# Kernel optimization log

Hardware: AMD Instinct MI355X
Metric: run time of the kernel (lower is better)

The kernel has to match this reference:

```python
import jax, jax.numpy as jnp
import numpy as np

EMBED_DIM = 1024
NUM_HEADS = 16
HEAD_DIM = EMBED_DIM // NUM_HEADS


def setup_inputs() -> dict:
    key = jax.random.key(0)
    k_x, k_wqkv, k_bqkv, k_wout, k_bout = jax.random.split(key, 5)
    s = 1.0 / np.sqrt(EMBED_DIM)
    return {
        "x": jax.random.normal(k_x, (2, 2048, EMBED_DIM), dtype=jnp.float32),
        "w_qkv": jax.random.uniform(k_wqkv, (EMBED_DIM, 3 * EMBED_DIM), jnp.float32, -s, s),
        "b_qkv": jax.random.uniform(k_bqkv, (3 * EMBED_DIM,), jnp.float32, -s, s),
        "w_out": jax.random.uniform(k_wout, (EMBED_DIM, EMBED_DIM), jnp.float32, -s, s),
        "b_out": jax.random.uniform(k_bout, (EMBED_DIM,), jnp.float32, -s, s),
    }


def reference(x, w_qkv, b_qkv, w_out, b_out):
    B, S, D = x.shape
    H, Hd = NUM_HEADS, HEAD_DIM
    # qkv projection, then per-head chunk: layout matches torch view(B,S,H,3*Hd).chunk(3,-1)
    qkv = (x @ w_qkv + b_qkv).reshape(B, S, H, 3, Hd)  # [B,S,H,3,Hd]
    q = qkv[..., 0, :]  # [B,S,H,Hd]
    k = qkv[..., 1, :]
    v = qkv[..., 2, :]
    scale = 1.0 / np.sqrt(Hd).astype(np.float32)
    scores = jnp.einsum("bqhd,bkhd->bhqk", q, k) * scale  # [B,H,S,S]
    probs = jax.nn.softmax(scores, axis=-1)
    out = jnp.einsum("bhqk,bkhd->bqhd", probs, v).reshape(B, S, D)
    return out @ w_out + b_out
```

## Files before the change

kernel.cpp:

```cpp
#include <hip/hip_runtime.h>
#include <hip/hip_bf16.h>


typedef __bf16 bf16;
typedef __bf16 bf16x8 __attribute__((ext_vector_type(8)));
typedef float  f32x4  __attribute__((ext_vector_type(4)));
typedef float  f32x16 __attribute__((ext_vector_type(16)));
typedef unsigned int uint;
typedef unsigned int uint2v __attribute__((ext_vector_type(2)));

__device__ __forceinline__ void gload_lds16(const void* g, void* l) {
  __builtin_amdgcn_global_load_lds(
      (const __attribute__((address_space(1))) unsigned int*)g,
      (__attribute__((address_space(3))) unsigned int*)l, 16, 0, 0);
}

__device__ __forceinline__ uint pkbf16(float lo, float hi) {
  union { bf16 h[2]; uint u; } t;
  t.h[0] = (bf16)lo; t.h[1] = (bf16)hi;
  return t.u;
}

__device__ __forceinline__ void pl32swapu(uint& a, uint& b) {
  uint2v r = __builtin_amdgcn_permlane32_swap(a, b, false, false);
  a = r.x; b = r.y;
}
__device__ __forceinline__ void pl32swapf(float& a, float& b) {
  uint ua = __builtin_bit_cast(uint, a), ub = __builtin_bit_cast(uint, b);
  pl32swapu(ua, ub);
  a = __builtin_bit_cast(float, ua); b = __builtin_bit_cast(float, ub);
}

__global__ __launch_bounds__(256) void k_prep(const float* __restrict__ x,
                                              const float* __restrict__ w_qkv,
                                              const float* __restrict__ w_out,
                                              bf16* __restrict__ xb,
                                              bf16* __restrict__ wqT,
                                              bf16* __restrict__ woT) {
  __shared__ float tile[32][33];
  const int b = blockIdx.x;
  const int tid = threadIdx.x;
  if (b < 2048) {
    int i = (b * 256 + tid) * 8;
    float4 a = *(const float4*)(x + i);
    float4 c = *(const float4*)(x + i + 4);
    bf16x8 o;
    o[0] = (bf16)a.x; o[1] = (bf16)a.y; o[2] = (bf16)a.z; o[3] = (bf16)a.w;
    o[4] = (bf16)c.x; o[5] = (bf16)c.y; o[6] = (bf16)c.z; o[7] = (bf16)c.w;
    *(bf16x8*)(xb + i) = o;
    return;
  }
  const bool perm = (b < 5120);
  const float* in = perm ? w_qkv : w_out;
  bf16* out = perm ? wqT : woT;
  const int N = perm ? 3072 : 1024;
  int idx = perm ? (b - 2048) : (b - 5120);
  int gx = perm ? (idx % 96) : (idx % 32);
  int gy = perm ? (idx / 96) : (idx / 32);
  int n0 = gx * 32, k0 = gy * 32;
  int tx = tid & 31, ty = tid >> 5;
#pragma unroll
  for (int i = 0; i < 4; i++)
    tile[ty + i * 8][tx] = in[(size_t)(k0 + ty + i * 8) * N + n0 + tx];
  __syncthreads();
#pragma unroll
  for (int i = 0; i < 4; i++) {
    int n = n0 + ty + i * 8;
    int row = n;
    if (perm) {
      int rem = n % 192;
      row = (rem >> 6) * 1024 + (n / 192) * 64 + (rem & 63);
    }
    out[(size_t)row * 1024 + k0 + tx] = (bf16)tile[tx][ty + i * 8];
  }
}

template<int BM, int BN>
__device__ __forceinline__ void gemm_tile(const bf16* __restrict__ A, const bf16* __restrict__ B,
                                          int K, int m0, int n0,
                                          bf16* As, bf16* Bs, f32x4 acc[BM / 32][BN / 32]) {
  const int tid  = threadIdx.x;
  const int lane = tid & 63;
  const int wr   = (tid >> 7) & 1;
  const int wc   = (tid >> 6) & 1;
  constexpr int LA = BM / 64, LB = BN / 64;
  auto stage = [&](int k0v, int b) {
#pragma unroll
    for (int i = 0; i < LA; i++) {
      int row = i * 64 + (tid >> 2);
      int sw  = (tid & 3) ^ (row & 3);
      gload_lds16(A + (size_t)(m0 + row) * K + k0v + sw * 8, (char*)As + b * (BM * 64) + i * 4096 + tid * 16);
    }
#pragma unroll
    for (int i = 0; i < LB; i++) {
      int row = i * 64 + (tid >> 2);
      int sw  = (tid & 3) ^ (row & 3);
      gload_lds16(B + (size_t)(n0 + row) * K + k0v + sw * 8, (char*)Bs + b * (BN * 64) + i * 4096 + tid * 16);
    }
  };
  const int nk = K / 32;
  stage(0, 0); stage(32, 1); stage(64, 2);
  for (int t = 0; t < nk; t++) {
    if (t < nk - 2) {
      if constexpr (LA + LB == 4) asm volatile("s_waitcnt vmcnt(8)" ::: "memory");
      else                        asm volatile("s_waitcnt vmcnt(6)" ::: "memory");
    } else if (t < nk - 1) {
      if constexpr (LA + LB == 4) asm volatile("s_waitcnt vmcnt(4)" ::: "memory");
      else                        asm volatile("s_waitcnt vmcnt(3)" ::: "memory");
    } else {
      asm volatile("s_waitcnt vmcnt(0)" ::: "memory");
    }
    __builtin_amdgcn_s_barrier();
    asm volatile("" ::: "memory");
    if (t + 3 < nk) stage((t + 3) * 32, (t + 3) & 3);
    const int cur = t & 3;
    bf16x8 af[BM / 32], bfr[BN / 32];
#pragma unroll
    for (int r = 0; r < BM / 32; r++) {
      int ra = wr * (BM / 2) + r * 16 + (lane & 15);
      af[r]  = *(const bf16x8*)((const char*)As + cur * (BM * 64) + ra * 64 + ((((lane >> 4) << 4)) ^ ((ra & 3) << 4)));
    }
#pragma unroll
    for (int c = 0; c < BN / 32; c++) {
      int rb = wc * (BN / 2) + c * 16 + (lane & 15);
      bfr[c] = *(const bf16x8*)((const char*)Bs + cur * (BN * 64) + rb * 64 + ((((lane >> 4) << 4)) ^ ((rb & 3) << 4)));
    }
#pragma unroll
    for (int r = 0; r < BM / 32; r++)
#pragma unroll
      for (int c = 0; c < BN / 32; c++)
        acc[r][c] = __builtin_amdgcn_mfma_f32_16x16x32_bf16(af[r], bfr[c], acc[r][c], 0, 0, 0);
    asm volatile("" ::: "memory");
  }
}

__global__ __launch_bounds__(512, 2) void k_gemm_qkv(const bf16* __restrict__ A, const bf16* __restrict__ Bt,
                                                     const float* __restrict__ bias,
                                                     bf16* __restrict__ qb, char* __restrict__ kf,
                                                     char* __restrict__ vf) {
  __shared__ char GS[131072];
  const int tid  = threadIdx.x;
  const int lane = tid & 63;
  const int wave = tid >> 6;
  const int wr   = wave >> 2;
  const int wc   = wave & 3;
  const int l = blockIdx.x;
  const int swz = (l & 7) * 24 + (l >> 3);
  const int m0 = (swz / 12) * 256, n0 = (swz % 12) * 256;
  const int K = 1024;

  f32x4 acc[8][4];
  f32x4 zero = {0.f, 0.f, 0.f, 0.f};
#pragma unroll
  for (int ms = 0; ms < 8; ms++)
#pragma unroll
    for (int ns = 0; ns < 4; ns++) acc[ms][ns] = zero;

  const int ccs = tid & 7;
  int rA[2], rB[2];
  {
    int lr0 = tid >> 3;
    rA[0] = lr0;
    rB[0] = (lr0 & 31) + ((lr0 >> 5) << 6);
    int lr1 = 64 + lr0;
    rA[1] = (lr1 & 63) + 128;
    rB[1] = (lr1 & 31) + ((lr1 >> 5) << 6);
  }
  const bf16* Agp[2]; const bf16* Bgp[2];
  int Alo[2], Blo[2];
#pragma unroll
  for (int j = 0; j < 2; j++) {
    Agp[j] = A  + (size_t)(m0 + rA[j]) * K + (ccs ^ (rA[j] & 7)) * 8;
    Alo[j] = rA[j] * 128 + ccs * 16;
    Bgp[j] = Bt + (size_t)(n0 + rB[j]) * K + (ccs ^ (rB[j] & 7)) * 8;
    Blo[j] = rB[j] * 128 + ccs * 16;
  }
  auto stA = [&](int t, int h) {
    int b = t & 1;
#pragma unroll
    for (int j = 0; j < 2; j++)
      gload_lds16(Agp[j] + (size_t)(h * 64) * K + t * 64, GS + b * 32768 + Alo[j] + h * 8192);
  };
  auto stB = [&](int t, int h) {
    int b = t & 1;
#pragma unroll
    for (int j = 0; j < 2; j++)
      gload_lds16(Bgp[j] + (size_t)(h * 32) * K + t * 64, GS + 65536 + b * 32768 + Blo[j] + h * 4096);
  };

  bf16x8 af[4][2], bf0[2][2], bf1[2][2];
  auto rdA = [&](const char* Ab, int mh) {
#pragma unroll
    for (int ms = 0; ms < 4; ms++)
#pragma unroll
      for (int ks = 0; ks < 2; ks++) {
        int row = wr * 128 + (mh * 4 + ms) * 16 + (lane & 15);
        int ch = (ks * 4 + (lane >> 4)) ^ (row & 7);
        af[ms][ks] = *(const bf16x8*)(Ab + row * 128 + ch * 16);
      }
  };
  auto rdB = [&](const char* Bb, int nh, bf16x8 (&bfx)[2][2]) {
#pragma unroll
    for (int ns = 0; ns < 2; ns++)
#pragma unroll
      for (int ks = 0; ks < 2; ks++) {
        int row = wc * 64 + (nh * 2 + ns) * 16 + (lane & 15);
        int ch = (ks * 4 + (lane >> 4)) ^ (row & 7);
        bfx[ns][ks] = *(const bf16x8*)(Bb + row * 128 + ch * 16);
      }
  };
  auto mm = [&](int mh, int nh, bf16x8 (&bfx)[2][2]) {
    __builtin_amdgcn_s_setprio(1);
#pragma unroll
    for (int ks = 0; ks < 2; ks++)
#pragma unroll
      for (int ms = 0; ms < 4; ms++)
#pragma unroll
        for (int ns = 0; ns < 2; ns++)
          acc[mh * 4 + ms][nh * 2 + ns] =
              __builtin_amdgcn_mfma_f32_16x16x32_bf16(af[ms][ks], bfx[ns][ks],
                                                      acc[mh * 4 + ms][nh * 2 + ns], 0, 0, 0);
    __builtin_amdgcn_s_setprio(0);
  };

#define BARRIER do { asm volatile("" ::: "memory"); __builtin_amdgcn_s_barrier(); \
                     asm volatile("" ::: "memory"); } while (0)

  stA(0, 0); stB(0, 0); stB(0, 1); stA(0, 1);
  stA(1, 0); stB(1, 0); stB(1, 1);
  asm volatile("s_waitcnt vmcnt(6)" ::: "memory");
  __builtin_amdgcn_s_barrier();
  asm volatile("" ::: "memory");

  for (int I = 0; I < 8; I++) {
    const int T = 2 * I;
    const char* Ab0 = GS;
    const char* Bb0 = GS + 65536;
    const char* Ab1 = GS + 32768;
    const char* Bb1 = GS + 65536 + 32768;
    const bool m2 = (T + 2 < 16), m3 = (T + 3 < 16);

    rdA(Ab0, 0); rdB(Bb0, 0, bf0);
    stA(T + 1, 1);
    BARRIER;
    mm(0, 0, bf0);

    rdB(Bb0, 1, bf1);
    if (m2) stA(T + 2, 0);
    BARRIER;
    mm(0, 1, bf1);

    rdA(Ab0, 1);
    if (m2) stB(T + 2, 0);
    BARRIER;
    mm(1, 0, bf0);

    if (m2) {
      stB(T + 2, 1);
      asm volatile("s_waitcnt vmcnt(6)" ::: "memory");
    } else {
      asm volatile("s_waitcnt vmcnt(0)" ::: "memory");
    }
    __builtin_amdgcn_s_barrier();
    asm volatile("" ::: "memory");
    mm(1, 1, bf1);

    rdA(Ab1, 0); rdB(Bb1, 0, bf0);
    if (m2) stA(T + 2, 1);
    BARRIER;
    mm(0, 0, bf0);

    rdB(Bb1, 1, bf1);
    if (m3) stA(T + 3, 0);
    BARRIER;
    mm(0, 1, bf1);

    rdA(Ab1, 1);
    if (m3) stB(T + 3, 0);
    BARRIER;
    mm(1, 0, bf0);

    if (m3) {
      stB(T + 3, 1);
      asm volatile("s_waitcnt vmcnt(6)" ::: "memory");
    } else {
      asm volatile("s_waitcnt vmcnt(0)" ::: "memory");
    }
    __builtin_amdgcn_s_barrier();
    asm volatile("" ::: "memory");
    mm(1, 1, bf1);
  }
#undef BARRIER

  const int group = n0 >> 10;
  const int hb = (n0 & 1023) >> 6;
  const int b_ = m0 >> 11;
  const int kt0 = (m0 & 2047) >> 5;
  const float QSs = 0.125f * 1.4426950408889634f;
  char* TL = GS;

  if (group < 2) {
#pragma unroll
    for (int ms = 0; ms < 8; ms++) {
      int mloc = wr * 128 + ms * 16 + ((lane >> 4) << 2);
#pragma unroll
      for (int ns = 0; ns < 4; ns++) {
        int nloc = wc * 64 + ns * 16 + (lane & 15);
        int np = n0 + nloc;
        float bv = bias[((np & 1023) >> 6) * 192 + group * 64 + (np & 63)];
#pragma unroll
        for (int g = 0; g < 4; g++) {
          float v = acc[ms][ns][g] + bv;
          if (group == 0) v *= QSs;
          int m = mloc + g;
          int byte = m * 512 + ((((nloc >> 3) ^ (m & 7)) << 4) | ((nloc & 7) << 1));
          *(bf16*)(TL + byte) = (bf16)v;
        }
      }
    }
    __syncthreads();
    if (group == 0) {
#pragma unroll
      for (int it = 0; it < 16; it++) {
        int cid = it * 512 + tid;
        int row = cid >> 5, cc = cid & 31;
        int hh = hb + (cc >> 3), ck = cc & 7;
        bf16x8 v8 = *(const bf16x8*)(TL + row * 512 + ((cc ^ (row & 7)) << 4));
        *(bf16x8*)(qb + ((size_t)(b_ * 16 + hh) * 2048 + (m0 & 2047) + row) * 64 + ck * 8) = v8;
      }
    } else {
#pragma unroll
      for (int it = 0; it < 16; it++) {
        int cid = it * 512 + tid;
        int hh = cid >> 11;
        int ktl = (cid >> 8) & 7;
        int dc = (cid >> 6) & 3;
        int gg = (cid >> 5) & 1;
        int ln = cid & 31;
        int row = ktl * 32 + ln;
        int cc = hh * 8 + dc * 2 + gg;
        bf16x8 v8 = *(const bf16x8*)(TL + row * 512 + ((cc ^ (row & 7)) << 4));
        *(bf16x8*)(kf + ((size_t)(b_ * 16 + hb + hh) * 64 + kt0 + ktl) * 4096
                      + (dc * 2 + gg) * 512 + ln * 16) = v8;
      }
    }
  } else {
#pragma unroll
    for (int ms = 0; ms < 8; ms++) {
      int mloc = wr * 128 + ms * 16 + ((lane >> 4) << 2);
#pragma unroll
      for (int ns = 0; ns < 4; ns++) {
        int nloc = wc * 64 + ns * 16 + (lane & 15);
        int np = n0 + nloc;
        float bv = bias[((np & 1023) >> 6) * 192 + 2 * 64 + (np & 63)];
#pragma unroll
        for (int g = 0; g < 4; g++) {
          float v = acc[ms][ns][g] + bv;
          int m = mloc + g;
          int byte = nloc * 512 + ((((m >> 3) ^ (nloc & 7)) << 4) | ((m & 7) << 1));
          *(bf16*)(TL + byte) = (bf16)v;
        }
      }
    }
    __syncthreads();
#pragma unroll
    for (int it = 0; it < 16; it++) {
      int cid = it * 512 + tid;
      int hh = cid >> 11;
      int ktl = (cid >> 8) & 7;
      int kc = (cid >> 7) & 1;
      int dt = (cid >> 6) & 1;
      int gg = (cid >> 5) & 1;
      int ln = cid & 31;
      int row = hh * 64 + dt * 32 + ln;
      int mc = ktl * 4 + kc * 2 + gg;
      bf16x8 v8 = *(const bf16x8*)(TL + row * 512 + ((mc ^ (row & 7)) << 4));
      *(bf16x8*)(vf + ((size_t)(b_ * 16 + hb + hh) * 64 + kt0 + ktl) * 4096
                    + ((kc * 2 + dt) * 2 + gg) * 512 + ln * 16) = v8;
    }
  }
}

__global__ __launch_bounds__(256) void k_gemm_out(const bf16* __restrict__ A, const bf16* __restrict__ Bt,
                                                  const float* __restrict__ bias,
                                                  float* __restrict__ out) {
  __shared__ bf16 As[4 * 64 * 32];
  __shared__ bf16 Bs[4 * 128 * 32];
  const int l = blockIdx.x;
  const int swz = (l & 7) * 64 + (l >> 3);
  int m0 = (swz >> 3) * 64, n0 = (swz & 7) * 128;
  f32x4 zero = {0.f, 0.f, 0.f, 0.f};
  f32x4 acc[2][4];
#pragma unroll
  for (int r = 0; r < 2; r++)
#pragma unroll
    for (int c = 0; c < 4; c++) acc[r][c] = zero;
  gemm_tile<64, 128>(A, Bt, 1024, m0, n0, As, Bs, acc);
  const int lane = threadIdx.x & 63;
  const int wr = (threadIdx.x >> 7) & 1, wc = (threadIdx.x >> 6) & 1;
#pragma unroll
  for (int r = 0; r < 2; r++) {
    int mbase = m0 + wr * 32 + r * 16 + ((lane >> 4) << 2);
#pragma unroll
    for (int c = 0; c < 4; c++) {
      int n = n0 + wc * 64 + c * 16 + (lane & 15);
      float bv = bias[n];
#pragma unroll
      for (int g = 0; g < 4; g++)
        out[(size_t)(mbase + g) * 1024 + n] = acc[r][c][g] + bv;
    }
  }
}

__global__ __launch_bounds__(512, 2) void k_attn(const bf16* __restrict__ qb, const char* __restrict__ kf,
                                                 const char* __restrict__ vf, bf16* __restrict__ ob) {
  __shared__ char SMEM[73728];
  const int tid  = threadIdx.x;
  const int lane = tid & 63;
  const int wave = tid >> 6;
  const int qp   = wave & 3;
  const int half = wave >> 2;
  const int ln31 = lane & 31;
  const int g    = lane >> 5;

  int l = blockIdx.x;
  int x = l & 7, j = l >> 3;
  int qt = j & 7;
  int bh = x * 4 + (j >> 3);

  const int q0 = qt * 256 + qp * 64;

  bf16x8 qfa[4], qfb[4];
  {
    const bf16* qpa = qb + ((size_t)bh * 2048 + q0 + ln31) * 64 + g * 8;
    const bf16* qpb = qb + ((size_t)bh * 2048 + q0 + 32 + ln31) * 64 + g * 8;
#pragma unroll
    for (int dc = 0; dc < 4; dc++) {
      qfa[dc] = *(const bf16x8*)(qpa + dc * 16);
      qfb[dc] = *(const bf16x8*)(qpb + dc * 16);
    }
  }

  const f32x16 z16 = 0.f;
  f32x16 Oa0 = 0.f, Oa1 = 0.f, Ob0 = 0.f, Ob1 = 0.f;
  float lacc_a[4] = {0.f, 0.f, 0.f, 0.f};
  float lacc_b[4] = {0.f, 0.f, 0.f, 0.f};

  const int lb = (g * 32 + ln31) * 16;
  const char* Kp = kf + (size_t)bh * 262144 + (half * 32) * 4096 + lb;
  const char* Vp = vf + (size_t)bh * 262144 + (half * 32) * 4096 + lb;

  auto smx = [&](f32x16& sv, bf16x8& f0, bf16x8& f1, float (&lc)[4]) {
#pragma unroll
    for (int r = 0; r < 16; r++) sv[r] = __builtin_amdgcn_exp2f(sv[r]);
#pragma unroll
    for (int r = 0; r < 4; r++)
      lc[r] += (sv[r] + sv[r + 4]) + (sv[r + 8] + sv[r + 12]);
    uint a0 = pkbf16(sv[0], sv[1]), a1 = pkbf16(sv[2], sv[3]);
    uint a2 = pkbf16(sv[4], sv[5]), a3 = pkbf16(sv[6], sv[7]);
    pl32swapu(a0, a2); pl32swapu(a1, a3);
    union { uint w[4]; bf16x8 v; } pa;
    pa.w[0] = a0; pa.w[1] = a1; pa.w[2] = a2; pa.w[3] = a3;
    f0 = pa.v;
    uint b0 = pkbf16(sv[8], sv[9]),  b1 = pkbf16(sv[10], sv[11]);
    uint b2 = pkbf16(sv[12], sv[13]), b3 = pkbf16(sv[14], sv[15]);
    pl32swapu(b0, b2); pl32swapu(b1, b3);
    union { uint w[4]; bf16x8 v; } pb;
    pb.w[0] = b0; pb.w[1] = b1; pb.w[2] = b2; pb.w[3] = b3;
    f1 = pb.v;
  };

  bf16x8 k0 = *(const bf16x8*)(Kp +    0);
  bf16x8 k1 = *(const bf16x8*)(Kp + 1024);
  bf16x8 k2 = *(const bf16x8*)(Kp + 2048);
  bf16x8 k3 = *(const bf16x8*)(Kp + 3072);

  for (int ss = 0; ss < 32; ss++, Kp += 4096, Vp += 4096) {
    bf16x8 v00 = *(const bf16x8*)(Vp +    0);
    bf16x8 v01 = *(const bf16x8*)(Vp + 1024);
    bf16x8 v10 = *(const bf16x8*)(Vp + 2048);
    bf16x8 v11 = *(const bf16x8*)(Vp + 3072);
    bf16x8 n0 = *(const bf16x8*)(Kp + 4096);
    bf16x8 n1 = *(const bf16x8*)(Kp + 5120);
    bf16x8 n2 = *(const bf16x8*)(Kp + 6144);
    bf16x8 n3 = *(const bf16x8*)(Kp + 7168);

    f32x16 sa, sb;
    __builtin_amdgcn_s_setprio(1);
    sa = __builtin_amdgcn_mfma_f32_32x32x16_bf16(k0, qfa[0], z16, 0, 0, 0);
    sb = __builtin_amdgcn_mfma_f32_32x32x16_bf16(k0, qfb[0], z16, 0, 0, 0);
    sa = __builtin_amdgcn_mfma_f32_32x32x16_bf16(k1, qfa[1], sa, 0, 0, 0);
    sb = __builtin_amdgcn_mfma_f32_32x32x16_bf16(k1, qfb[1], sb, 0, 0, 0);
    sa = __builtin_amdgcn_mfma_f32_32x32x16_bf16(k2, qfa[2], sa, 0, 0, 0);
    sb = __builtin_amdgcn_mfma_f32_32x32x16_bf16(k2, qfb[2], sb, 0, 0, 0);
    sa = __builtin_amdgcn_mfma_f32_32x32x16_bf16(k3, qfa[3], sa, 0, 0, 0);
    sb = __builtin_amdgcn_mfma_f32_32x32x16_bf16(k3, qfb[3], sb, 0, 0, 0);
    __builtin_amdgcn_s_setprio(0);

    bf16x8 fa0, fa1, fb0, fb1;
    smx(sa, fa0, fa1, lacc_a);
    smx(sb, fb0, fb1, lacc_b);

    __builtin_amdgcn_s_setprio(1);
    Oa0 = __builtin_amdgcn_mfma_f32_32x32x16_bf16(v00, fa0, Oa0, 0, 0, 0);
    Ob0 = __builtin_amdgcn_mfma_f32_32x32x16_bf16(v00, fb0, Ob0, 0, 0, 0);
    Oa1 = __builtin_amdgcn_mfma_f32_32x32x16_bf16(v01, fa0, Oa1, 0, 0, 0);
    Ob1 = __builtin_amdgcn_mfma_f32_32x32x16_bf16(v01, fb0, Ob1, 0, 0, 0);
    Oa0 = __builtin_amdgcn_mfma_f32_32x32x16_bf16(v10, fa1, Oa0, 0, 0, 0);
    Ob0 = __builtin_amdgcn_mfma_f32_32x32x16_bf16(v10, fb1, Ob0, 0, 0, 0);
    Oa1 = __builtin_amdgcn_mfma_f32_32x32x16_bf16(v11, fa1, Oa1, 0, 0, 0);
    Ob1 = __builtin_amdgcn_mfma_f32_32x32x16_bf16(v11, fb1, Ob1, 0, 0, 0);
    __builtin_amdgcn_s_setprio(0);

    k0 = n0; k1 = n1; k2 = n2; k3 = n3;
  }

  float l_ra = (lacc_a[0] + lacc_a[1]) + (lacc_a[2] + lacc_a[3]);
  { float o = l_ra; pl32swapf(l_ra, o); l_ra += o; }
  float l_rb = (lacc_b[0] + lacc_b[1]) + (lacc_b[2] + lacc_b[3]);
  { float o = l_rb; pl32swapf(l_rb, o); l_rb += o; }

  float* Opart = (float*)SMEM;
  float* LsA   = (float*)(SMEM + 69632);
  float* LsB   = (float*)(SMEM + 70144);
  __syncthreads();
  if (half == 1) {
    float* my = Opart + (qp * 64 + lane) * 68;
#pragma unroll
    for (int c = 0; c < 4; c++) {
      *(f32x4*)(my +      c * 4) = f32x4{Oa0[c*4], Oa0[c*4+1], Oa0[c*4+2], Oa0[c*4+3]};
      *(f32x4*)(my + 16 + c * 4) = f32x4{Oa1[c*4], Oa1[c*4+1], Oa1[c*4+2], Oa1[c*4+3]};
      *(f32x4*)(my + 32 + c * 4) = f32x4{Ob0[c*4], Ob0[c*4+1], Ob0[c*4+2], Ob0[c*4+3]};
      *(f32x4*)(my + 48 + c * 4) = f32x4{Ob1[c*4], Ob1[c*4+1], Ob1[c*4+2], Ob1[c*4+3]};
    }
    if (lane < 32) { LsA[qp * 32 + ln31] = l_ra; LsB[qp * 32 + ln31] = l_rb; }
  }
  __syncthreads();
  float inva = 0.f, invb = 0.f;
  if (half == 0) {
    const float* pr = Opart + (qp * 64 + lane) * 68;
#pragma unroll
    for (int c = 0; c < 4; c++) {
      f32x4 a0 = *(const f32x4*)(pr +      c * 4);
      f32x4 a1 = *(const f32x4*)(pr + 16 + c * 4);
      f32x4 b0 = *(const f32x4*)(pr + 32 + c * 4);
      f32x4 b1 = *(const f32x4*)(pr + 48 + c * 4);
#pragma unroll
      for (int k = 0; k < 4; k++) {
        Oa0[c*4+k] += a0[k]; Oa1[c*4+k] += a1[k];
        Ob0[c*4+k] += b0[k]; Ob1[c*4+k] += b1[k];
      }
    }
    inva = 1.0f / (l_ra + LsA[qp * 32 + ln31]);
    invb = 1.0f / (l_rb + LsB[qp * 32 + ln31]);
  }
  __syncthreads();
  bf16 (*Os)[64][72] = reinterpret_cast<bf16 (*)[64][72]>(SMEM);
  if (half == 0) {
#pragma unroll
    for (int r = 0; r < 16; r++) {
      int d0 = (r & 3) + 8 * (r >> 2) + 4 * g;
      Os[qp][ln31][d0]           = (bf16)(Oa0[r] * inva);
      Os[qp][ln31][d0 + 32]      = (bf16)(Oa1[r] * inva);
      Os[qp][32 + ln31][d0]      = (bf16)(Ob0[r] * invb);
      Os[qp][32 + ln31][d0 + 32] = (bf16)(Ob1[r] * invb);
    }
  }
  __syncthreads();
  {
    int b_ = bh >> 4, h = bh & 15;
#pragma unroll
    for (int it = 0; it < 4; it++) {
      int cid = it * 512 + tid;
      int row256 = cid >> 3, c = cid & 7;
      int qpp = row256 >> 6, row = row256 & 63;
      bf16x8 v8o = *(const bf16x8*)&Os[qpp][row][c * 8];
      *(bf16x8*)(ob + ((size_t)(b_ * 2048 + qt * 256 + qpp * 64 + row)) * 1024 + h * 64 + c * 8) = v8o;
    }
  }
}

extern "C" void kernel_launch(void* const* d_in, const int* in_sizes, int n_in,
                              void* d_out, int out_size, void* d_ws, size_t ws_size,
                              hipStream_t stream) {
  const float* x     = (const float*)d_in[0];
  const float* w_qkv = (const float*)d_in[1];
  const float* b_qkv = (const float*)d_in[2];
  const float* w_out = (const float*)d_in[3];
  const float* b_out = (const float*)d_in[4];
  float* out = (float*)d_out;

  char* ws = (char*)d_ws;
  bf16* xb  = (bf16*)ws;
  bf16* wqT = (bf16*)(ws + (8ull  << 20));
  bf16* woT = (bf16*)(ws + (14ull << 20));
  bf16* qb  = (bf16*)(ws + (16ull << 20));
  char* kf  = ws + (24ull << 20);
  char* vf  = ws + (32ull << 20);

  k_prep<<<6144, 256, 0, stream>>>(x, w_qkv, w_out, xb, wqT, woT);
  k_gemm_qkv<<<192, 512, 0, stream>>>(xb, wqT, b_qkv, qb, kf, vf);
  k_attn<<<256, 512, 0, stream>>>(qb, kf, vf, xb);
  k_gemm_out<<<512, 256, 0, stream>>>(xb, woT, b_out, out);
}
```

Baseline: 103.6 us.

## Split attention KV range four ways per query tile and double grid size

Each attention block now covers 128 queries instead of 256, with 4 waves per query pair each taking a quarter of the KV sequence. Partial outputs and row sums are combined through shared memory in a two-step tree reduction. The grid doubles to 512 blocks so all CUs are filled, and the launch bound is raised to 4 blocks per CU. The cost is that Q fragments are loaded by more waves, there are more barriers and LDS traffic in the reduction, and register pressure rises under the tighter launch bound.

```diff
diff --git a/kernel.cpp b/kernel.cpp
--- a/kernel.cpp
+++ b/kernel.cpp
@@ -412,23 +412,23 @@
   }
 }
 
-__global__ __launch_bounds__(512, 2) void k_attn(const bf16* __restrict__ qb, const char* __restrict__ kf,
+__global__ __launch_bounds__(512, 4) void k_attn(const bf16* __restrict__ qb, const char* __restrict__ kf,
                                                  const char* __restrict__ vf, bf16* __restrict__ ob) {
   __shared__ char SMEM[73728];
   const int tid  = threadIdx.x;
   const int lane = tid & 63;
   const int wave = tid >> 6;
-  const int qp   = wave & 3;
-  const int half = wave >> 2;
+  const int qp   = wave & 1;
+  const int kvq  = wave >> 1;
   const int ln31 = lane & 31;
   const int g    = lane >> 5;
 
   int l = blockIdx.x;
   int x = l & 7, j = l >> 3;
-  int qt = j & 7;
-  int bh = x * 4 + (j >> 3);
-
-  const int q0 = qt * 256 + qp * 64;
+  int qt = j & 15;
+  int bh = x * 4 + (j >> 4);
+
+  const int q0 = qt * 128 + qp * 64;
 
   bf16x8 qfa[4], qfb[4];
   {
@@ -447,8 +447,8 @@
   float lacc_b[4] = {0.f, 0.f, 0.f, 0.f};
 
   const int lb = (g * 32 + ln31) * 16;
-  const char* Kp = kf + (size_t)bh * 262144 + (half * 32) * 4096 + lb;
-  const char* Vp = vf + (size_t)bh * 262144 + (half * 32) * 4096 + lb;
+  const char* Kp = kf + (size_t)bh * 262144 + (size_t)(kvq * 16) * 4096 + lb;
+  const char* Vp = vf + (size_t)bh * 262144 + (size_t)(kvq * 16) * 4096 + lb;
 
   auto smx = [&](f32x16& sv, bf16x8& f0, bf16x8& f1, float (&lc)[4]) {
 #pragma unroll
@@ -475,7 +475,7 @@
   bf16x8 k2 = *(const bf16x8*)(Kp + 2048);
   bf16x8 k3 = *(const bf16x8*)(Kp + 3072);
 
-  for (int ss = 0; ss < 32; ss++, Kp += 4096, Vp += 4096) {
+  for (int ss = 0; ss < 16; ss++, Kp += 4096, Vp += 4096) {
     bf16x8 v00 = *(const bf16x8*)(Vp +    0);
     bf16x8 v01 = *(const bf16x8*)(Vp + 1024);
     bf16x8 v10 = *(const bf16x8*)(Vp + 2048);
@@ -521,11 +521,9 @@
   { float o = l_rb; pl32swapf(l_rb, o); l_rb += o; }
 
   float* Opart = (float*)SMEM;
-  float* LsA   = (float*)(SMEM + 69632);
-  float* LsB   = (float*)(SMEM + 70144);
-  __syncthreads();
-  if (half == 1) {
-    float* my = Opart + (qp * 64 + lane) * 68;
+  float* Ls    = (float*)(SMEM + 69632);
+  auto writeO = [&](int slot) {
+    float* my = Opart + (slot * 64 + lane) * 68;
 #pragma unroll
     for (int c = 0; c < 4; c++) {
       *(f32x4*)(my +      c * 4) = f32x4{Oa0[c*4], Oa0[c*4+1], Oa0[c*4+2], Oa0[c*4+3]};
@@ -533,12 +531,10 @@
       *(f32x4*)(my + 32 + c * 4) = f32x4{Ob0[c*4], Ob0[c*4+1], Ob0[c*4+2], Ob0[c*4+3]};
       *(f32x4*)(my + 48 + c * 4) = f32x4{Ob1[c*4], Ob1[c*4+1], Ob1[c*4+2], Ob1[c*4+3]};
     }
-    if (lane < 32) { LsA[qp * 32 + ln31] = l_ra; LsB[qp * 32 + ln31] = l_rb; }
-  }
-  __syncthreads();
-  float inva = 0.f, invb = 0.f;
-  if (half == 0) {
-    const float* pr = Opart + (qp * 64 + lane) * 68;
+    if (lane < 32) { Ls[(slot * 2 + 0) * 32 + ln31] = l_ra; Ls[(slot * 2 + 1) * 32 + ln31] = l_rb; }
+  };
+  auto addO = [&](int slot) {
+    const float* pr = Opart + (slot * 64 + lane) * 68;
 #pragma unroll
     for (int c = 0; c < 4; c++) {
       f32x4 a0 = *(const f32x4*)(pr +      c * 4);
@@ -551,12 +547,26 @@
         Ob0[c*4+k] += b0[k]; Ob1[c*4+k] += b1[k];
       }
     }
-    inva = 1.0f / (l_ra + LsA[qp * 32 + ln31]);
-    invb = 1.0f / (l_rb + LsB[qp * 32 + ln31]);
+    l_ra += Ls[(slot * 2 + 0) * 32 + ln31];
+    l_rb += Ls[(slot * 2 + 1) * 32 + ln31];
+  };
+
+  __syncthreads();
+  if (kvq >= 2) writeO(qp * 2 + (kvq - 2));
+  __syncthreads();
+  if (kvq < 2) addO(qp * 2 + kvq);
+  __syncthreads();
+  if (kvq == 1) writeO(qp);
+  __syncthreads();
+  float inva = 0.f, invb = 0.f;
+  if (kvq == 0) {
+    addO(qp);
+    inva = 1.0f / l_ra;
+    invb = 1.0f / l_rb;
   }
   __syncthreads();
   bf16 (*Os)[64][72] = reinterpret_cast<bf16 (*)[64][72]>(SMEM);
-  if (half == 0) {
+  if (kvq == 0) {
 #pragma unroll
     for (int r = 0; r < 16; r++) {
       int d0 = (r & 3) + 8 * (r >> 2) + 4 * g;
@@ -570,12 +580,12 @@
   {
     int b_ = bh >> 4, h = bh & 15;
 #pragma unroll
-    for (int it = 0; it < 4; it++) {
+    for (int it = 0; it < 2; it++) {
       int cid = it * 512 + tid;
-      int row256 = cid >> 3, c = cid & 7;
-      int qpp = row256 >> 6, row = row256 & 63;
+      int row128 = cid >> 3, c = cid & 7;
+      int qpp = row128 >> 6, row = row128 & 63;
       bf16x8 v8o = *(const bf16x8*)&Os[qpp][row][c * 8];
-      *(bf16x8*)(ob + ((size_t)(b_ * 2048 + qt * 256 + qpp * 64 + row)) * 1024 + h * 64 + c * 8) = v8o;
+      *(bf16x8*)(ob + ((size_t)(b_ * 2048 + qt * 128 + row128)) * 1024 + h * 64 + c * 8) = v8o;
     }
   }
 }
@@ -600,6 +610,6 @@
 
   k_prep<<<6144, 256, 0, stream>>>(x, w_qkv, w_out, xb, wqT, woT);
   k_gemm_qkv<<<192, 512, 0, stream>>>(xb, wqT, b_qkv, qb, kf, vf);
-  k_attn<<<256, 512, 0, stream>>>(qb, kf, vf, xb);
+  k_attn<<<512, 512, 0, stream>>>(qb, kf, vf, xb);
   k_gemm_out<<<512, 256, 0, stream>>>(xb, woT, b_out, out);
 }
```

After: 279.5 us. 2.7x slower.

## Software-pipeline attention loop so QK of next tile overlaps PV of current

Applied to the files above, without the earlier changes.

Restructures the attention inner loop so the QK^T MFMAs for key tile i+1 are issued alongside the PV MFMAs for tile i, with the softmax exp/pack of the next scores done after. The first tile is peeled into a prologue and the last iteration skips QK. This is meant to hide the exp/pack VALU latency behind matrix work. It also drops the occupancy hint of 2 from launch bounds, which lets the compiler use more registers for the extra live values at possible cost in occupancy.

```diff
diff --git a/kernel.cpp b/kernel.cpp
--- a/kernel.cpp
+++ b/kernel.cpp
@@ -412,8 +412,8 @@
   }
 }
 
-__global__ __launch_bounds__(512, 2) void k_attn(const bf16* __restrict__ qb, const char* __restrict__ kf,
-                                                 const char* __restrict__ vf, bf16* __restrict__ ob) {
+__global__ __launch_bounds__(512) void k_attn(const bf16* __restrict__ qb, const char* __restrict__ kf,
+                                              const char* __restrict__ vf, bf16* __restrict__ ob) {
   __shared__ char SMEM[73728];
   const int tid  = threadIdx.x;
   const int lane = tid & 63;
@@ -447,8 +447,8 @@
   float lacc_b[4] = {0.f, 0.f, 0.f, 0.f};
 
   const int lb = (g * 32 + ln31) * 16;
-  const char* Kp = kf + (size_t)bh * 262144 + (half * 32) * 4096 + lb;
-  const char* Vp = vf + (size_t)bh * 262144 + (half * 32) * 4096 + lb;
+  const char* Kb = kf + (size_t)bh * 262144 + (size_t)(half * 32) * 4096 + lb;
+  const char* Vb = vf + (size_t)bh * 262144 + (size_t)(half * 32) * 4096 + lb;
 
   auto smx = [&](f32x16& sv, bf16x8& f0, bf16x8& f1, float (&lc)[4]) {
 #pragma unroll
@@ -470,38 +470,47 @@
     f1 = pb.v;
   };
 
-  bf16x8 k0 = *(const bf16x8*)(Kp +    0);
-  bf16x8 k1 = *(const bf16x8*)(Kp + 1024);
-  bf16x8 k2 = *(const bf16x8*)(Kp + 2048);
-  bf16x8 k3 = *(const bf16x8*)(Kp + 3072);
-
-  for (int ss = 0; ss < 32; ss++, Kp += 4096, Vp += 4096) {
-    bf16x8 v00 = *(const bf16x8*)(Vp +    0);
-    bf16x8 v01 = *(const bf16x8*)(Vp + 1024);
-    bf16x8 v10 = *(const bf16x8*)(Vp + 2048);
-    bf16x8 v11 = *(const bf16x8*)(Vp + 3072);
-    bf16x8 n0 = *(const bf16x8*)(Kp + 4096);
-    bf16x8 n1 = *(const bf16x8*)(Kp + 5120);
-    bf16x8 n2 = *(const bf16x8*)(Kp + 6144);
-    bf16x8 n3 = *(const bf16x8*)(Kp + 7168);
-
+  bf16x8 k0, k1, k2, k3, v00, v01, v10, v11;
+  bf16x8 fa0, fa1, fb0, fb1;
+  {
+    bf16x8 p0 = *(const bf16x8*)(Kb +    0);
+    bf16x8 p1 = *(const bf16x8*)(Kb + 1024);
+    bf16x8 p2 = *(const bf16x8*)(Kb + 2048);
+    bf16x8 p3 = *(const bf16x8*)(Kb + 3072);
+    f32x16 sa, sb;
+    sa = __builtin_amdgcn_mfma_f32_32x32x16_bf16(p0, qfa[0], z16, 0, 0, 0);
+    sb = __builtin_amdgcn_mfma_f32_32x32x16_bf16(p0, qfb[0], z16, 0, 0, 0);
+    sa = __builtin_amdgcn_mfma_f32_32x32x16_bf16(p1, qfa[1], sa, 0, 0, 0);
+    sb = __builtin_amdgcn_mfma_f32_32x32x16_bf16(p1, qfb[1], sb, 0, 0, 0);
+    sa = __builtin_amdgcn_mfma_f32_32x32x16_bf16(p2, qfa[2], sa, 0, 0, 0);
+    sb = __builtin_amdgcn_mfma_f32_32x32x16_bf16(p2, qfb[2], sb, 0, 0, 0);
+    sa = __builtin_amdgcn_mfma_f32_32x32x16_bf16(p3, qfa[3], sa, 0, 0, 0);
+    sb = __builtin_amdgcn_mfma_f32_32x32x16_bf16(p3, qfb[3], sb, 0, 0, 0);
+    smx(sa, fa0, fa1, lacc_a);
+    smx(sb, fb0, fb1, lacc_b);
+  }
+  v00 = *(const bf16x8*)(Vb +    0);
+  v01 = *(const bf16x8*)(Vb + 1024);
+  v10 = *(const bf16x8*)(Vb + 2048);
+  v11 = *(const bf16x8*)(Vb + 3072);
+  k0 = *(const bf16x8*)(Kb + 4096);
+  k1 = *(const bf16x8*)(Kb + 5120);
+  k2 = *(const bf16x8*)(Kb + 6144);
+  k3 = *(const bf16x8*)(Kb + 7168);
+
+  for (int ss = 0; ss < 32; ss++) {
     f32x16 sa, sb;
     __builtin_amdgcn_s_setprio(1);
-    sa = __builtin_amdgcn_mfma_f32_32x32x16_bf16(k0, qfa[0], z16, 0, 0, 0);
-    sb = __builtin_amdgcn_mfma_f32_32x32x16_bf16(k0, qfb[0], z16, 0, 0, 0);
-    sa = __builtin_amdgcn_mfma_f32_32x32x16_bf16(k1, qfa[1], sa, 0, 0, 0);
-    sb = __builtin_amdgcn_mfma_f32_32x32x16_bf16(k1, qfb[1], sb, 0, 0, 0);
-    sa = __builtin_amdgcn_mfma_f32_32x32x16_bf16(k2, qfa[2], sa, 0, 0, 0);
-    sb = __builtin_amdgcn_mfma_f32_32x32x16_bf16(k2, qfb[2], sb, 0, 0, 0);
-    sa = __builtin_amdgcn_mfma_f32_32x32x16_bf16(k3, qfa[3], sa, 0, 0, 0);
-    sb = __builtin_amdgcn_mfma_f32_32x32x16_bf16(k3, qfb[3], sb, 0, 0, 0);
-    __builtin_amdgcn_s_setprio(0);
-
-    bf16x8 fa0, fa1, fb0, fb1;
-    smx(sa, fa0, fa1, lacc_a);
-    smx(sb, fb0, fb1, lacc_b);
-
-    __builtin_amdgcn_s_setprio(1);
+    if (ss < 31) {
+      sa = __builtin_amdgcn_mfma_f32_32x32x16_bf16(k0, qfa[0], z16, 0, 0, 0);
+      sb = __builtin_amdgcn_mfma_f32_32x32x16_bf16(k0, qfb[0], z16, 0, 0, 0);
+      sa = __builtin_amdgcn_mfma_f32_32x32x16_bf16(k1, qfa[1], sa, 0, 0, 0);
+      sb = __builtin_amdgcn_mfma_f32_32x32x16_bf16(k1, qfb[1], sb, 0, 0, 0);
+      sa = __builtin_amdgcn_mfma_f32_32x32x16_bf16(k2, qfa[2], sa, 0, 0, 0);
+      sb = __builtin_amdgcn_mfma_f32_32x32x16_bf16(k2, qfb[2], sb, 0, 0, 0);
+      sa = __builtin_amdgcn_mfma_f32_32x32x16_bf16(k3, qfa[3], sa, 0, 0, 0);
+      sb = __builtin_amdgcn_mfma_f32_32x32x16_bf16(k3, qfb[3], sb, 0, 0, 0);
+    }
     Oa0 = __builtin_amdgcn_mfma_f32_32x32x16_bf16(v00, fa0, Oa0, 0, 0, 0);
     Ob0 = __builtin_amdgcn_mfma_f32_32x32x16_bf16(v00, fb0, Ob0, 0, 0, 0);
     Oa1 = __builtin_amdgcn_mfma_f32_32x32x16_bf16(v01, fa0, Oa1, 0, 0, 0);
@@ -512,7 +521,19 @@
     Ob1 = __builtin_amdgcn_mfma_f32_32x32x16_bf16(v11, fb1, Ob1, 0, 0, 0);
     __builtin_amdgcn_s_setprio(0);
 
-    k0 = n0; k1 = n1; k2 = n2; k3 = n3;
+    if (ss < 31) {
+      v00 = *(const bf16x8*)(Vb + 4096 +    0);
+      v01 = *(const bf16x8*)(Vb + 4096 + 1024);
+      v10 = *(const bf16x8*)(Vb + 4096 + 2048);
+      v11 = *(const bf16x8*)(Vb + 4096 + 3072);
+      k0 = *(const bf16x8*)(Kb + 8192 +    0);
+      k1 = *(const bf16x8*)(Kb + 8192 + 1024);
+      k2 = *(const bf16x8*)(Kb + 8192 + 2048);
+      k3 = *(const bf16x8*)(Kb + 8192 + 3072);
+      Kb += 4096; Vb += 4096;
+      smx(sa, fa0, fa1, lacc_a);
+      smx(sb, fb0, fb1, lacc_b);
+    }
   }
 
   float l_ra = (lacc_a[0] + lacc_a[1]) + (lacc_a[2] + lacc_a[3]);
```

Measured after the change: 108.7 us. 4.8% more time.
